# Kernel optimization log

Hardware: AMD Instinct MI355X
Metric: run time of the kernel (lower is better)

## Reference

```python
import jax, jax.numpy as jnp
import numpy as np

B, N, D_IN, H, NH = 8, 1024, 3072, 128, 4
DH = H // NH
LN_EPS = 1e-5


def make_mask(key, p):
    A = jax.random.bernoulli(key, p, (N, N)).astype(jnp.float32)
    A_tilde = A + jnp.eye(N, dtype=jnp.float32)  # add self-loops
    return jnp.where(A_tilde > 0, 0.0, -jnp.inf).astype(jnp.float32)


def setup_inputs() -> dict:
    key = jax.random.key(0)
    ks = jax.random.split(key, 20)
    s = 0.02
    inp = {
        "stim_features": jax.random.normal(ks[0], (B, D_IN), jnp.float32),
        # stim encoder
        "W_enc1": jax.random.normal(ks[1], (2 * H, D_IN), jnp.float32) * s,
        "b_enc1": jnp.zeros((2 * H,), jnp.float32),
        "ln_g": jnp.ones((2 * H,), jnp.float32),
        "ln_b": jnp.zeros((2 * H,), jnp.float32),
        "W_enc2": jax.random.normal(ks[2], (H, 2 * H), jnp.float32) * s,
        "b_enc2": jnp.zeros((H,), jnp.float32),
        "voxel_emb": jax.random.normal(ks[3], (N, H), jnp.float32) * 0.01,
        # GAT projection weights (Linear, no bias), [out, in]
        "W_func1": jax.random.normal(ks[4], (H, H), jnp.float32) * s,
        "W_roi1": jax.random.normal(ks[5], (H, H), jnp.float32) * s,
        "W_func2": jax.random.normal(ks[6], (H, H), jnp.float32) * s,
        "W_roi2": jax.random.normal(ks[7], (H, H), jnp.float32) * s,
        # fusion / skip / readout
        "W_fu1": jax.random.normal(ks[8], (H, 2 * H), jnp.float32) * s,
        "b_fu1": jnp.zeros((H,), jnp.float32),
        "W_fu2": jax.random.normal(ks[9], (H, 2 * H), jnp.float32) * s,
        "b_fu2": jnp.zeros((H,), jnp.float32),
        "W_sk1": jax.random.normal(ks[10], (H, H), jnp.float32) * s,
        "b_sk1": jnp.zeros((H,), jnp.float32),
        "W_sk2": jax.random.normal(ks[11], (H, H), jnp.float32) * s,
        "b_sk2": jnp.zeros((H,), jnp.float32),
        "W_ro": jax.random.normal(ks[12], (1, H), jnp.float32) * s,
        "b_ro": jnp.zeros((1,), jnp.float32),
        # static adjacency masks (buffers, 0 / -inf)
        "mask_func": make_mask(ks[13], 0.01),
        "mask_roi": make_mask(ks[14], 0.05),
    }
    return inp


def gat(h, W, mask):
    # h: [B, N, H]; W: [H, H]; mask: [N, N]
    Bq, Nq, _ = h.shape
    Wh = (h @ W.T).reshape(Bq, Nq, NH, DH).transpose(0, 2, 1, 3)  # [B, nh, N, dh]
    scores = jnp.einsum("bhnd,bhmd->bhnm", Wh, Wh) / np.sqrt(DH)
    scores = scores + mask[None, None]
    attn = jax.nn.softmax(scores, axis=-1)  # dropout = identity (eval mode)
    hp = jnp.einsum("bhnm,bhmd->bhnd", attn, Wh)
    hp = hp.transpose(0, 2, 1, 3).reshape(Bq, Nq, NH * DH)
    return jax.nn.elu(hp)


def reference(stim_features, W_enc1, b_enc1, ln_g, ln_b, W_enc2, b_enc2,
              voxel_emb, W_func1, W_roi1, W_func2, W_roi2,
              W_fu1, b_fu1, W_fu2, b_fu2, W_sk1, b_sk1, W_sk2, b_sk2,
              W_ro, b_ro, mask_func, mask_roi):
    # stim encoder: Linear -> LayerNorm -> GELU -> Linear (dropout = identity)
    z = stim_features @ W_enc1.T + b_enc1
    mu = jnp.mean(z, axis=-1, keepdims=True)
    var = jnp.var(z, axis=-1, keepdims=True)
    z = (z - mu) * jax.lax.rsqrt(var + LN_EPS) * ln_g + ln_b
    z = jax.nn.gelu(z, approximate=False)
    g = z @ W_enc2.T + b_enc2  # [B, H]

    x = g[:, None, :] + voxel_emb[None]  # [B, N, H]
    x_res1 = x
    h1 = jnp.concatenate([gat(x, W_func1, mask_func), gat(x, W_roi1, mask_roi)], axis=-1)
    x = h1 @ W_fu1.T + b_fu1
    x = x + (x_res1 @ W_sk1.T + b_sk1)
    x_res2 = x
    h2 = jnp.concatenate([gat(x, W_func2, mask_func), gat(x, W_roi2, mask_roi)], axis=-1)
    x = h2 @ W_fu2.T + b_fu2
    x = x + (x_res2 @ W_sk2.T + b_sk2)
    pred = (x @ W_ro.T + b_ro)[..., 0]  # [B, N]
    return pred
```

## Files before the change

### kernel.cpp

```cpp
#include <hip/hip_runtime.h>
#include <hip/hip_bf16.h>
#include <math.h>

#define B_SZ 8
#define N_SZ 1024
#define D_IN 3072
#define H_SZ 128
#define NH 4
#define DH 32
#define TWO_H 256
#define LN_EPS 1e-5f
#define CAP 128

typedef __attribute__((ext_vector_type(8))) short bf16x8;
typedef __attribute__((ext_vector_type(8))) unsigned short u16x8;
typedef __attribute__((ext_vector_type(4))) float f32x4;
typedef __attribute__((ext_vector_type(4))) unsigned int u32x4;

__device__ inline unsigned short f2bf(float f) {
    unsigned int u = __builtin_bit_cast(unsigned int, f);
    u += 0x7fffu + ((u >> 16) & 1u);
    return (unsigned short)(u >> 16);
}

__global__ __launch_bounds__(256) void prep_kernel(
        const float* __restrict__ Wfu1, const float* __restrict__ Wsk1,
        const float* __restrict__ Wfu2, const float* __restrict__ Wsk2,
        const float* __restrict__ Wf1, const float* __restrict__ Wr1,
        const float* __restrict__ Wf2, const float* __restrict__ Wr2,
        unsigned short* __restrict__ wb,
        const float* __restrict__ m0, const float* __restrict__ m1,
        int* __restrict__ i0, int* __restrict__ i1,
        int* __restrict__ d0, int* __restrict__ d1,
        const float* __restrict__ stim, const float* __restrict__ W1,
        const float* __restrict__ b1, float* __restrict__ z) {
    const int bid = blockIdx.x;
    const int tid = threadIdx.x;

    if (bid < 128) {
        const int j = bid;
        wb[j * 384 + tid] = f2bf(Wfu1[j * 256 + tid]);
        wb[49152 + j * 384 + tid] = f2bf(Wfu2[j * 256 + tid]);
        if (tid < 128) {
            wb[j * 384 + 256 + tid]         = f2bf(Wsk1[j * 128 + tid]);
            wb[49152 + j * 384 + 256 + tid] = f2bf(Wsk2[j * 128 + tid]);
            wb[98304  + j * 128 + tid] = f2bf(Wf1[j * 128 + tid]);
            wb[114688 + j * 128 + tid] = f2bf(Wr1[j * 128 + tid]);
            wb[131072 + j * 128 + tid] = f2bf(Wf2[j * 128 + tid]);
            wb[147456 + j * 128 + tid] = f2bf(Wr2[j * 128 + tid]);
        }
    } else if (bid < 640) {
        const int bIdx = bid - 128;
        const int gsel = bIdx >> 8;
        const float* mask = gsel ? m1 : m0;
        int* idx = gsel ? i1 : i0;
        int* deg = gsel ? d1 : d0;
        const int row = (bIdx & 255) * 4 + (tid >> 6);
        const int lane = tid & 63;
        const float* mrow = mask + (size_t)row * N_SZ;
        int* irow = idx + (size_t)row * CAP;

        int base = 0;
        #pragma unroll 4
        for (int t = 0; t < N_SZ / 64; ++t) {
            int c = t * 64 + lane;
            bool edge = (mrow[c] == 0.0f);
            unsigned long long ball = __ballot(edge);
            unsigned long long below = ball & ((1ull << lane) - 1ull);
            if (edge) {
                int p = base + __popcll(below);
                if (p < CAP) irow[p] = c;
            }
            base += __popcll(ball);
        }
        if (lane == 0) deg[row] = (base < CAP) ? base : CAP;
    } else {
        const int j = bid - 640;
        const float4* w4 = (const float4*)(W1 + (size_t)j * D_IN);
        const float4* s4 = (const float4*)stim;

        float acc[B_SZ];
        #pragma unroll
        for (int b = 0; b < B_SZ; ++b) acc[b] = 0.0f;

        #pragma unroll
        for (int i = 0; i < D_IN / 4 / 256; ++i) {
            const int k4 = tid + i * 256;
            const float4 w = w4[k4];
            #pragma unroll
            for (int b = 0; b < B_SZ; ++b) {
                const float4 s = s4[b * (D_IN / 4) + k4];
                acc[b] += s.x * w.x + s.y * w.y + s.z * w.z + s.w * w.w;
            }
        }
        #pragma unroll
        for (int b = 0; b < B_SZ; ++b) {
            float v = acc[b];
            v += __shfl_xor(v, 1);  v += __shfl_xor(v, 2);  v += __shfl_xor(v, 4);
            v += __shfl_xor(v, 8);  v += __shfl_xor(v, 16); v += __shfl_xor(v, 32);
            acc[b] = v;
        }
        __shared__ float red[4][B_SZ];
        const int wave = tid >> 6, lane = tid & 63;
        if (lane == 0) {
            #pragma unroll
            for (int b = 0; b < B_SZ; ++b) red[wave][b] = acc[b];
        }
        __syncthreads();
        if (tid < B_SZ) {
            float v = red[0][tid] + red[1][tid] + red[2][tid] + red[3][tid];
            z[tid * TWO_H + j] = v + b1[j];
        }
    }
}

__global__ __launch_bounds__(256) void enc23_kernel(
        const float* __restrict__ z,
        const float* __restrict__ lng, const float* __restrict__ lnb,
        const float* __restrict__ W2, const float* __restrict__ b2,
        float* __restrict__ g) {
    __shared__ float red[TWO_H];
    __shared__ float zgs[TWO_H];
    __shared__ float gp[2][H_SZ];
    const int b = blockIdx.x;
    const int tid = threadIdx.x;

    float zi = z[b * TWO_H + tid];
    red[tid] = zi; __syncthreads();
    for (int s = 128; s > 0; s >>= 1) { if (tid < s) red[tid] += red[tid + s]; __syncthreads(); }
    float mu = red[0] * (1.0f / TWO_H);
    __syncthreads();
    float dz = zi - mu;
    red[tid] = dz * dz; __syncthreads();
    for (int s = 128; s > 0; s >>= 1) { if (tid < s) red[tid] += red[tid + s]; __syncthreads(); }
    float var = red[0] * (1.0f / TWO_H);

    float zn = dz * (1.0f / sqrtf(var + LN_EPS)) * lng[tid] + lnb[tid];
    zgs[tid] = 0.5f * zn * (1.0f + erff(zn * 0.70710678118654752f));
    __syncthreads();

    const int j = tid & 127, half = tid >> 7;
    const float* w2r = W2 + (size_t)j * TWO_H + half * 128;
    const float* zh = &zgs[half * 128];
    float s = 0.0f;
    #pragma unroll 4
    for (int k = 0; k < 128; ++k) s += zh[k] * w2r[k];
    gp[half][j] = s;
    __syncthreads();
    if (tid < H_SZ) g[b * H_SZ + tid] = gp[0][tid] + gp[1][tid] + b2[tid];
}

template<int NSEG, bool OB16, bool AEMB, bool RO, bool AB16>
__global__ __launch_bounds__(256) void gemm_mfma(
        const void* __restrict__ a0, const void* __restrict__ a1,
        const void* __restrict__ a2,
        const float* __restrict__ gvec, const float* __restrict__ emb,
        const unsigned short* __restrict__ wba, const unsigned short* __restrict__ wbb,
        const float* __restrict__ bias1, const float* __restrict__ bias2,
        void* __restrict__ outa, void* __restrict__ outb,
        const float* __restrict__ Wro, const float* __restrict__ bro,
        float* __restrict__ pred) {
    const unsigned short* wb = blockIdx.y ? wbb : wba;
    void* out = blockIdx.y ? outb : outa;
    const int KW = NSEG * 128;

    __shared__ __align__(16) short As[32 * 128];
    __shared__ __align__(16) short Bs[64 * 128];
    __shared__ float part[2][32];

    const int bid = blockIdx.x;
    const int ct = bid & 1, rt = bid >> 1;
    const int row0 = rt * 32, col0 = ct * 64;
    const int tid = threadIdx.x;
    const int lane = tid & 63, w = tid >> 6;
    const int wm = w >> 1, wn = w & 1;
    const int lrow = lane & 15, lk = lane >> 4;

    f32x4 acc0 = {0.f, 0.f, 0.f, 0.f};
    f32x4 acc1 = {0.f, 0.f, 0.f, 0.f};

    for (int seg = 0; seg < NSEG; ++seg) {
        const void* src = (seg == 0) ? a0 : ((seg == 1) ? a1 : a2);
        const bool useEmb = AEMB && (NSEG == 1 || seg == 2);
        if (seg) __syncthreads();
        for (int gi = tid; gi < 512; gi += 256) {
            const int r = gi >> 4, kq = gi & 15;
            u16x8 t;
            if (useEmb) {
                const int row = row0 + r;
                const float4* gp = (const float4*)(gvec + (size_t)(row >> 10) * H_SZ) + kq * 2;
                const float4* ep = (const float4*)(emb + (size_t)(row & 1023) * H_SZ) + kq * 2;
                const float4 g0 = gp[0], g1 = gp[1], e0 = ep[0], e1 = ep[1];
                t[0] = f2bf(g0.x + e0.x); t[1] = f2bf(g0.y + e0.y);
                t[2] = f2bf(g0.z + e0.z); t[3] = f2bf(g0.w + e0.w);
                t[4] = f2bf(g1.x + e1.x); t[5] = f2bf(g1.y + e1.y);
                t[6] = f2bf(g1.z + e1.z); t[7] = f2bf(g1.w + e1.w);
            } else if (AB16) {
                t = *(const u16x8*)((const unsigned short*)src
                                    + (size_t)(row0 + r) * H_SZ + kq * 8);
            } else {
                const float4* sp = (const float4*)((const float*)src
                                    + (size_t)(row0 + r) * H_SZ) + kq * 2;
                const float4 v0 = sp[0], v1 = sp[1];
                t[0] = f2bf(v0.x); t[1] = f2bf(v0.y); t[2] = f2bf(v0.z); t[3] = f2bf(v0.w);
                t[4] = f2bf(v1.x); t[5] = f2bf(v1.y); t[6] = f2bf(v1.z); t[7] = f2bf(v1.w);
            }
            *(u16x8*)&As[r * 128 + ((kq * 8) ^ ((r & 7) << 3))] = t;
        }
        for (int gi = tid; gi < 1024; gi += 256) {
            const int c = gi >> 4, kq = gi & 15;
            const float4 v = *(const float4*)(wb + (size_t)(col0 + c) * KW + seg * 128 + kq * 8);
            *(float4*)&Bs[c * 128 + ((kq * 8) ^ ((c & 7) << 3))] = v;
        }
        __syncthreads();

        #pragma unroll
        for (int ks = 0; ks < 4; ++ks) {
            const int kof = ks * 32 + lk * 8;
            const int r = wm * 16 + lrow;
            const bf16x8 a = *(const bf16x8*)&As[r * 128 + (kof ^ ((r & 7) << 3))];
            const int c0 = wn * 32 + lrow;
            const bf16x8 b0 = *(const bf16x8*)&Bs[c0 * 128 + (kof ^ ((c0 & 7) << 3))];
            const int c1 = c0 + 16;
            const bf16x8 b1 = *(const bf16x8*)&Bs[c1 * 128 + (kof ^ ((c1 & 7) << 3))];
            acc0 = __builtin_amdgcn_mfma_f32_16x16x32_bf16(a, b0, acc0, 0, 0, 0);
            acc1 = __builtin_amdgcn_mfma_f32_16x16x32_bf16(a, b1, acc1, 0, 0, 0);
        }
    }

    const int rb = row0 + wm * 16 + lk * 4;
    if constexpr (RO) {
        float pr[4] = {0.f, 0.f, 0.f, 0.f};
        #pragma unroll
        for (int fc = 0; fc < 2; ++fc) {
            const int c = col0 + wn * 32 + fc * 16 + lrow;
            const float bias = bias1[c] + bias2[c];
            const float wro = Wro[c];
            const f32x4 a = fc ? acc1 : acc0;
            #pragma unroll
            for (int rr = 0; rr < 4; ++rr) pr[rr] += (a[rr] + bias) * wro;
        }
        #pragma unroll
        for (int rr = 0; rr < 4; ++rr) {
            pr[rr] += __shfl_xor(pr[rr], 1);
            pr[rr] += __shfl_xor(pr[rr], 2);
            pr[rr] += __shfl_xor(pr[rr], 4);
            pr[rr] += __shfl_xor(pr[rr], 8);
        }
        if (lrow == 0) {
            #pragma unroll
            for (int rr = 0; rr < 4; ++rr) part[wn][wm * 16 + lk * 4 + rr] = pr[rr];
        }
        __syncthreads();
        if (tid < 32) {
            float v = part[0][tid] + part[1][tid];
            if (ct == 0) v += bro[0];
            atomicAdd(pred + row0 + tid, v);
        }
    } else {
        #pragma unroll
        for (int fc = 0; fc < 2; ++fc) {
            const int c = col0 + wn * 32 + fc * 16 + lrow;
            const float bias = (bias1 ? bias1[c] : 0.0f) + (bias2 ? bias2[c] : 0.0f);
            const f32x4 a = fc ? acc1 : acc0;
            #pragma unroll
            for (int rr = 0; rr < 4; ++rr) {
                if constexpr (OB16) {
                    ((unsigned short*)out)[(size_t)(rb + rr) * H_SZ + c] = f2bf(a[rr] + bias);
                } else {
                    ((float*)out)[(size_t)(rb + rr) * H_SZ + c] = a[rr] + bias;
                }
            }
        }
    }
}

__global__ __launch_bounds__(256) void attn_kernel(
        const unsigned short* __restrict__ Wha, const unsigned short* __restrict__ Whb,
        const int* __restrict__ ia, const int* __restrict__ ib,
        const int* __restrict__ da, const int* __restrict__ db,
        unsigned short* __restrict__ oa, unsigned short* __restrict__ ob) {
    const unsigned short* Wh = blockIdx.y ? Whb : Wha;
    const int* idx = blockIdx.y ? ib : ia;
    const int* deg = blockIdx.y ? db : da;
    unsigned short* out = blockIdx.y ? ob : oa;

    const int bid = blockIdx.x;
    const int b = bid & 7;
    const int i = ((bid >> 3) << 2) | (threadIdx.x >> 6);
    const int bi = b * N_SZ + i;
    const int lane = threadIdx.x & 63;
    const int c = lane & 15;
    const int e4 = lane >> 4;

    const u32x4 qb = *(const u32x4*)(Wh + (size_t)bi * H_SZ + c * 8);
    float qf[8];
    #pragma unroll
    for (int m = 0; m < 4; ++m) {
        qf[2 * m]     = __builtin_bit_cast(float, qb[m] << 16) * 0.25505654741110714f;
        qf[2 * m + 1] = __builtin_bit_cast(float, qb[m] & 0xffff0000u) * 0.25505654741110714f;
    }

    const int dg = deg[i];
    const int* row = idx + (size_t)i * CAP;
    int idxv0 = row[lane] & 1023;
    int idxv1 = (dg > 64) ? (row[64 + lane] & 1023) : 0;

    const unsigned short* kbase = Wh + (size_t)b * N_SZ * H_SZ;

    float acc[8];
    #pragma unroll
    for (int k = 0; k < 8; ++k) acc[k] = 0.0f;
    float l = 0.0f;

    auto loadSeg = [&](int s, u32x4* kv) {
        const int srcv = (s >= 4) ? idxv1 : idxv0;
        const int off16 = (s & 3) << 4;
        #pragma unroll
        for (int t = 0; t < 4; ++t) {
            const int j0 = __builtin_amdgcn_readlane(srcv, off16 + 4 * t);
            const int j1 = __builtin_amdgcn_readlane(srcv, off16 + 4 * t + 1);
            const int j2 = __builtin_amdgcn_readlane(srcv, off16 + 4 * t + 2);
            const int j3 = __builtin_amdgcn_readlane(srcv, off16 + 4 * t + 3);
            const int jlo = (e4 & 1) ? j1 : j0;
            const int jhi = (e4 & 1) ? j3 : j2;
            const int j = (e4 & 2) ? jhi : jlo;
            kv[t] = *(const u32x4*)(kbase + (size_t)j * H_SZ + c * 8);
        }
    };
    auto computeSeg = [&](int s, const u32x4* kv) {
        const int ebase = s << 4;
        #pragma unroll
        for (int t = 0; t < 4; ++t) {
            float kf[8];
            #pragma unroll
            for (int m = 0; m < 4; ++m) {
                kf[2 * m]     = __builtin_bit_cast(float, kv[t][m] << 16);
                kf[2 * m + 1] = __builtin_bit_cast(float, kv[t][m] & 0xffff0000u);
            }
            float s2 = 0.0f;
            #pragma unroll
            for (int k = 0; k < 8; ++k) s2 += qf[k] * kf[k];
            s2 += __shfl_xor(s2, 1);
            s2 += __shfl_xor(s2, 2);
            const bool valid = (ebase + 4 * t + e4) < dg;
            const float p = valid ? __builtin_amdgcn_exp2f(s2) : 0.0f;
            l += p;
            #pragma unroll
            for (int k = 0; k < 8; ++k) acc[k] += p * kf[k];
        }
    };

    const int nseg = (dg + 15) >> 4;
    u32x4 kvA[4], kvB[4];
    loadSeg(0, kvA);
    int seg = 0;
    while (true) {
        if (seg + 1 < nseg) loadSeg(seg + 1, kvB);
        computeSeg(seg, kvA);
        ++seg; if (seg >= nseg) break;
        if (seg + 1 < nseg) loadSeg(seg + 1, kvA);
        computeSeg(seg, kvB);
        ++seg; if (seg >= nseg) break;
    }

    l += __shfl_xor(l, 16);
    l += __shfl_xor(l, 32);
    #pragma unroll
    for (int k = 0; k < 8; ++k) {
        acc[k] += __shfl_xor(acc[k], 16);
        acc[k] += __shfl_xor(acc[k], 32);
    }

    if (e4 == 0) {
        const float inv = 1.0f / l;
        u16x8 ov;
        #pragma unroll
        for (int k = 0; k < 8; ++k) {
            const float hp = acc[k] * inv;
            const float o = (hp > 0.0f) ? hp
                 : (__builtin_amdgcn_exp2f(hp * 1.4426950408889634f) - 1.0f);
            ov[k] = f2bf(o);
        }
        *(u16x8*)(out + (size_t)bi * H_SZ + c * 8) = ov;
    }
}

extern "C" void kernel_launch(void* const* d_in, const int* in_sizes, int n_in,
                              void* d_out, int out_size, void* d_ws, size_t ws_size,
                              hipStream_t stream) {
    const float* stim   = (const float*)d_in[0];
    const float* W_enc1 = (const float*)d_in[1];
    const float* b_enc1 = (const float*)d_in[2];
    const float* ln_g   = (const float*)d_in[3];
    const float* ln_b   = (const float*)d_in[4];
    const float* W_enc2 = (const float*)d_in[5];
    const float* b_enc2 = (const float*)d_in[6];
    const float* vox    = (const float*)d_in[7];
    const float* W_f1   = (const float*)d_in[8];
    const float* W_r1   = (const float*)d_in[9];
    const float* W_f2   = (const float*)d_in[10];
    const float* W_r2   = (const float*)d_in[11];
    const float* W_fu1  = (const float*)d_in[12];
    const float* b_fu1  = (const float*)d_in[13];
    const float* W_fu2  = (const float*)d_in[14];
    const float* b_fu2  = (const float*)d_in[15];
    const float* W_sk1  = (const float*)d_in[16];
    const float* b_sk1  = (const float*)d_in[17];
    const float* W_sk2  = (const float*)d_in[18];
    const float* b_sk2  = (const float*)d_in[19];
    const float* W_ro   = (const float*)d_in[20];
    const float* b_ro   = (const float*)d_in[21];
    const float* mask_f = (const float*)d_in[22];
    const float* mask_r = (const float*)d_in[23];

    float* pred = (float*)d_out;

    float* ws  = (float*)d_ws;
    float* z   = ws;
    float* g   = z + 2048;
    unsigned short* x2_16 = (unsigned short*)(g + 1024);
    unsigned short* hf16  = x2_16 + 1048576;
    unsigned short* hr16  = hf16 + 1048576;
    unsigned short* Whf16 = hr16 + 1048576;
    unsigned short* Whr16 = Whf16 + 1048576;
    int* idxf  = (int*)(Whr16 + 1048576);
    int* idxr  = idxf + N_SZ * CAP;
    int* degf  = idxr + N_SZ * CAP;
    int* degr  = degf + N_SZ;
    unsigned short* wb16 = (unsigned short*)(degr + N_SZ);
    unsigned short* wcat1 = wb16;
    unsigned short* wcat2 = wb16 + 49152;
    unsigned short* wpf1  = wb16 + 98304;
    unsigned short* wpr1  = wb16 + 114688;
    unsigned short* wpf2  = wb16 + 131072;
    unsigned short* wpr2  = wb16 + 147456;

    const int BN = B_SZ * N_SZ;

    hipMemsetAsync(pred, 0, BN * sizeof(float), stream);

    prep_kernel<<<896, 256, 0, stream>>>(
        W_fu1, W_sk1, W_fu2, W_sk2, W_f1, W_r1, W_f2, W_r2, wb16,
        mask_f, mask_r, idxf, idxr, degf, degr,
        stim, W_enc1, b_enc1, z);
    enc23_kernel<<<B_SZ, 256, 0, stream>>>(z, ln_g, ln_b, W_enc2, b_enc2, g);

    gemm_mfma<1, true, true, false, false><<<dim3(BN / 32 * 2, 2), 256, 0, stream>>>(
        nullptr, nullptr, nullptr, g, vox, wpf1, wpr1, nullptr, nullptr,
        Whf16, Whr16, nullptr, nullptr, nullptr);
    attn_kernel<<<dim3(BN / 4, 2), 256, 0, stream>>>(Whf16, Whr16, idxf, idxr, degf, degr,
                                                     hf16, hr16);
    gemm_mfma<3, true, true, false, true><<<dim3(BN / 32 * 2, 1), 256, 0, stream>>>(
        hf16, hr16, nullptr, g, vox, wcat1, wcat1, b_fu1, b_sk1,
        x2_16, x2_16, nullptr, nullptr, nullptr);

    gemm_mfma<1, true, false, false, true><<<dim3(BN / 32 * 2, 2), 256, 0, stream>>>(
        x2_16, nullptr, nullptr, nullptr, nullptr, wpf2, wpr2, nullptr, nullptr,
        Whf16, Whr16, nullptr, nullptr, nullptr);
    attn_kernel<<<dim3(BN / 4, 2), 256, 0, stream>>>(Whf16, Whr16, idxf, idxr, degf, degr,
                                                     hf16, hr16);
    gemm_mfma<3, false, false, true, true><<<dim3(BN / 32 * 2, 1), 256, 0, stream>>>(
        hf16, hr16, x2_16, nullptr, nullptr, wcat2, wcat2, b_fu2, b_sk2,
        nullptr, nullptr, W_ro, b_ro, pred);
}
```

Measured before the change: 96.76 us.

## Fuse fusion GEMM with layer-2 projections and readout into per-row-tile kernels

Adds a kernel that computes the layer-1 fusion and skip output for a 16-row tile, keeps it in shared memory, and immediately applies both layer-2 GAT projections, replacing two GEMM launches. It also adds a final kernel that computes the layer-2 fusion and skip and reduces the readout dot product in-block, writing pred directly without atomics. This drops the pred memset and the round-trip of x2 between launches. In exchange, each block reloads the full 128x128 weight tiles for only 16 rows, which means much more weight traffic per row and only a single wave of MFMA work per block.

```diff
diff --git a/kernel.cpp b/kernel.cpp
--- a/kernel.cpp
+++ b/kernel.cpp
@@ -275,6 +275,190 @@
     }
 }
 
+__global__ __launch_bounds__(256) void fusproj_kernel(
+        const unsigned short* __restrict__ hf, const unsigned short* __restrict__ hr,
+        const float* __restrict__ gvec, const float* __restrict__ emb,
+        const unsigned short* __restrict__ wcat,
+        const float* __restrict__ bfu, const float* __restrict__ bsk,
+        const unsigned short* __restrict__ wpf, const unsigned short* __restrict__ wpr,
+        unsigned short* __restrict__ x2, unsigned short* __restrict__ whf,
+        unsigned short* __restrict__ whr) {
+    __shared__ __align__(16) short As[16 * 128];
+    __shared__ __align__(16) short Bs[128 * 128];
+    const int row0 = blockIdx.x * 16;
+    const int tid = threadIdx.x;
+    const int lane = tid & 63, w = tid >> 6;
+    const int lrow = lane & 15, lk = lane >> 4;
+
+    f32x4 acc0 = {0.f, 0.f, 0.f, 0.f};
+    f32x4 acc1 = {0.f, 0.f, 0.f, 0.f};
+
+    for (int seg = 0; seg < 3; ++seg) {
+        if (seg) __syncthreads();
+        {
+            const int r = tid >> 4, kq = tid & 15;
+            u16x8 t;
+            if (seg == 0) {
+                t = *(const u16x8*)(hf + (size_t)(row0 + r) * H_SZ + kq * 8);
+            } else if (seg == 1) {
+                t = *(const u16x8*)(hr + (size_t)(row0 + r) * H_SZ + kq * 8);
+            } else {
+                const int row = row0 + r;
+                const float4* gp = (const float4*)(gvec + (size_t)(row >> 10) * H_SZ) + kq * 2;
+                const float4* ep = (const float4*)(emb + (size_t)(row & 1023) * H_SZ) + kq * 2;
+                const float4 g0 = gp[0], g1 = gp[1], e0 = ep[0], e1 = ep[1];
+                t[0] = f2bf(g0.x + e0.x); t[1] = f2bf(g0.y + e0.y);
+                t[2] = f2bf(g0.z + e0.z); t[3] = f2bf(g0.w + e0.w);
+                t[4] = f2bf(g1.x + e1.x); t[5] = f2bf(g1.y + e1.y);
+                t[6] = f2bf(g1.z + e1.z); t[7] = f2bf(g1.w + e1.w);
+            }
+            *(u16x8*)&As[r * 128 + ((kq * 8) ^ ((r & 7) << 3))] = t;
+        }
+        for (int gi = tid; gi < 2048; gi += 256) {
+            const int c = gi >> 4, kq = gi & 15;
+            const float4 v = *(const float4*)(wcat + (size_t)c * 384 + seg * 128 + kq * 8);
+            *(float4*)&Bs[c * 128 + ((kq * 8) ^ ((c & 7) << 3))] = v;
+        }
+        __syncthreads();
+
+        #pragma unroll
+        for (int ks = 0; ks < 4; ++ks) {
+            const int kof = ks * 32 + lk * 8;
+            const bf16x8 a = *(const bf16x8*)&As[lrow * 128 + (kof ^ ((lrow & 7) << 3))];
+            const int c0 = w * 32 + lrow;
+            const bf16x8 b0 = *(const bf16x8*)&Bs[c0 * 128 + (kof ^ ((c0 & 7) << 3))];
+            const int c1 = c0 + 16;
+            const bf16x8 b1 = *(const bf16x8*)&Bs[c1 * 128 + (kof ^ ((c1 & 7) << 3))];
+            acc0 = __builtin_amdgcn_mfma_f32_16x16x32_bf16(a, b0, acc0, 0, 0, 0);
+            acc1 = __builtin_amdgcn_mfma_f32_16x16x32_bf16(a, b1, acc1, 0, 0, 0);
+        }
+    }
+    __syncthreads();
+
+    const int rb = lk * 4;
+    #pragma unroll
+    for (int fc = 0; fc < 2; ++fc) {
+        const int c = w * 32 + fc * 16 + lrow;
+        const float bias = bfu[c] + bsk[c];
+        const f32x4 a = fc ? acc1 : acc0;
+        #pragma unroll
+        for (int rr = 0; rr < 4; ++rr) {
+            const unsigned short v = f2bf(a[rr] + bias);
+            x2[(size_t)(row0 + rb + rr) * H_SZ + c] = v;
+            const int rl = rb + rr;
+            As[rl * 128 + (((c & ~7) ^ ((rl & 7) << 3)) | (c & 7))] = (short)v;
+        }
+    }
+    __syncthreads();
+
+    #pragma unroll
+    for (int gsel = 0; gsel < 2; ++gsel) {
+        const unsigned short* wp = gsel ? wpr : wpf;
+        unsigned short* out = gsel ? whr : whf;
+        if (gsel) __syncthreads();
+        for (int gi = tid; gi < 2048; gi += 256) {
+            const int c = gi >> 4, kq = gi & 15;
+            const float4 v = *(const float4*)(wp + (size_t)c * 128 + kq * 8);
+            *(float4*)&Bs[c * 128 + ((kq * 8) ^ ((c & 7) << 3))] = v;
+        }
+        __syncthreads();
+        f32x4 p0 = {0.f, 0.f, 0.f, 0.f};
+        f32x4 p1 = {0.f, 0.f, 0.f, 0.f};
+        #pragma unroll
+        for (int ks = 0; ks < 4; ++ks) {
+            const int kof = ks * 32 + lk * 8;
+            const bf16x8 a = *(const bf16x8*)&As[lrow * 128 + (kof ^ ((lrow & 7) << 3))];
+            const int c0 = w * 32 + lrow;
+            const bf16x8 b0 = *(const bf16x8*)&Bs[c0 * 128 + (kof ^ ((c0 & 7) << 3))];
+            const int c1 = c0 + 16;
+            const bf16x8 b1 = *(const bf16x8*)&Bs[c1 * 128 + (kof ^ ((c1 & 7) << 3))];
+            p0 = __builtin_amdgcn_mfma_f32_16x16x32_bf16(a, b0, p0, 0, 0, 0);
+            p1 = __builtin_amdgcn_mfma_f32_16x16x32_bf16(a, b1, p1, 0, 0, 0);
+        }
+        #pragma unroll
+        for (int fc = 0; fc < 2; ++fc) {
+            const int c = w * 32 + fc * 16 + lrow;
+            const f32x4 a = fc ? p1 : p0;
+            #pragma unroll
+            for (int rr = 0; rr < 4; ++rr)
+                out[(size_t)(row0 + rb + rr) * H_SZ + c] = f2bf(a[rr]);
+        }
+    }
+}
+
+__global__ __launch_bounds__(256) void fusro_kernel(
+        const unsigned short* __restrict__ hf, const unsigned short* __restrict__ hr,
+        const unsigned short* __restrict__ x2,
+        const unsigned short* __restrict__ wcat,
+        const float* __restrict__ bfu, const float* __restrict__ bsk,
+        const float* __restrict__ Wro, const float* __restrict__ bro,
+        float* __restrict__ pred) {
+    __shared__ __align__(16) short As[16 * 128];
+    __shared__ __align__(16) short Bs[128 * 128];
+    __shared__ float part[4][16];
+    const int row0 = blockIdx.x * 16;
+    const int tid = threadIdx.x;
+    const int lane = tid & 63, w = tid >> 6;
+    const int lrow = lane & 15, lk = lane >> 4;
+
+    f32x4 acc0 = {0.f, 0.f, 0.f, 0.f};
+    f32x4 acc1 = {0.f, 0.f, 0.f, 0.f};
+
+    for (int seg = 0; seg < 3; ++seg) {
+        if (seg) __syncthreads();
+        {
+            const int r = tid >> 4, kq = tid & 15;
+            const unsigned short* src = (seg == 0) ? hf : ((seg == 1) ? hr : x2);
+            const u16x8 t = *(const u16x8*)(src + (size_t)(row0 + r) * H_SZ + kq * 8);
+            *(u16x8*)&As[r * 128 + ((kq * 8) ^ ((r & 7) << 3))] = t;
+        }
+        for (int gi = tid; gi < 2048; gi += 256) {
+            const int c = gi >> 4, kq = gi & 15;
+            const float4 v = *(const float4*)(wcat + (size_t)c * 384 + seg * 128 + kq * 8);
+            *(float4*)&Bs[c * 128 + ((kq * 8) ^ ((c & 7) << 3))] = v;
+        }
+        __syncthreads();
+
+        #pragma unroll
+        for (int ks = 0; ks < 4; ++ks) {
+            const int kof = ks * 32 + lk * 8;
+            const bf16x8 a = *(const bf16x8*)&As[lrow * 128 + (kof ^ ((lrow & 7) << 3))];
+            const int c0 = w * 32 + lrow;
+            const bf16x8 b0 = *(const bf16x8*)&Bs[c0 * 128 + (kof ^ ((c0 & 7) << 3))];
+            const int c1 = c0 + 16;
+            const bf16x8 b1 = *(const bf16x8*)&Bs[c1 * 128 + (kof ^ ((c1 & 7) << 3))];
+            acc0 = __builtin_amdgcn_mfma_f32_16x16x32_bf16(a, b0, acc0, 0, 0, 0);
+            acc1 = __builtin_amdgcn_mfma_f32_16x16x32_bf16(a, b1, acc1, 0, 0, 0);
+        }
+    }
+
+    const int rb = lk * 4;
+    float pr[4] = {0.f, 0.f, 0.f, 0.f};
+    #pragma unroll
+    for (int fc = 0; fc < 2; ++fc) {
+        const int c = w * 32 + fc * 16 + lrow;
+        const float bias = bfu[c] + bsk[c];
+        const float wro = Wro[c];
+        const f32x4 a = fc ? acc1 : acc0;
+        #pragma unroll
+        for (int rr = 0; rr < 4; ++rr) pr[rr] += (a[rr] + bias) * wro;
+    }
+    #pragma unroll
+    for (int rr = 0; rr < 4; ++rr) {
+        pr[rr] += __shfl_xor(pr[rr], 1);
+        pr[rr] += __shfl_xor(pr[rr], 2);
+        pr[rr] += __shfl_xor(pr[rr], 4);
+        pr[rr] += __shfl_xor(pr[rr], 8);
+    }
+    if (lrow == 0) {
+        #pragma unroll
+        for (int rr = 0; rr < 4; ++rr) part[w][rb + rr] = pr[rr];
+    }
+    __syncthreads();
+    if (tid < 16)
+        pred[row0 + tid] = part[0][tid] + part[1][tid] + part[2][tid] + part[3][tid] + bro[0];
+}
+
 __global__ __launch_bounds__(256) void attn_kernel(
         const unsigned short* __restrict__ Wha, const unsigned short* __restrict__ Whb,
         const int* __restrict__ ia, const int* __restrict__ ib,
@@ -438,8 +622,6 @@
 
     const int BN = B_SZ * N_SZ;
 
-    hipMemsetAsync(pred, 0, BN * sizeof(float), stream);
-
     prep_kernel<<<896, 256, 0, stream>>>(
         W_fu1, W_sk1, W_fu2, W_sk2, W_f1, W_r1, W_f2, W_r2, wb16,
         mask_f, mask_r, idxf, idxr, degf, degr,
@@ -451,16 +633,12 @@
         Whf16, Whr16, nullptr, nullptr, nullptr);
     attn_kernel<<<dim3(BN / 4, 2), 256, 0, stream>>>(Whf16, Whr16, idxf, idxr, degf, degr,
                                                      hf16, hr16);
-    gemm_mfma<3, true, true, false, true><<<dim3(BN / 32 * 2, 1), 256, 0, stream>>>(
-        hf16, hr16, nullptr, g, vox, wcat1, wcat1, b_fu1, b_sk1,
-        x2_16, x2_16, nullptr, nullptr, nullptr);
-
-    gemm_mfma<1, true, false, false, true><<<dim3(BN / 32 * 2, 2), 256, 0, stream>>>(
-        x2_16, nullptr, nullptr, nullptr, nullptr, wpf2, wpr2, nullptr, nullptr,
-        Whf16, Whr16, nullptr, nullptr, nullptr);
+    fusproj_kernel<<<BN / 16, 256, 0, stream>>>(
+        hf16, hr16, g, vox, wcat1, b_fu1, b_sk1, wpf2, wpr2,
+        x2_16, Whf16, Whr16);
+
     attn_kernel<<<dim3(BN / 4, 2), 256, 0, stream>>>(Whf16, Whr16, idxf, idxr, degf, degr,
                                                      hf16, hr16);
-    gemm_mfma<3, false, false, true, true><<<dim3(BN / 32 * 2, 1), 256, 0, stream>>>(
-        hf16, hr16, x2_16, nullptr, nullptr, wcat2, wcat2, b_fu2, b_sk2,
-        nullptr, nullptr, W_ro, b_ro, pred);
-}
+    fusro_kernel<<<BN / 16, 256, 0, stream>>>(
+        hf16, hr16, x2_16, wcat2, b_fu2, b_sk2, W_ro, b_ro, pred);
+}
```

After: 88.21 us. 1.1x faster.
